# Kernel tuning notes

Measured on AMD Instinct MI355X. Metric: run time of the kernel, lower is better.

## Reference

```python
import jax, jax.numpy as jnp
import numpy as np

T, B, D, H, L = 512, 128, 256, 256, 4
EPS = 1e-5

def _ln(x, g, b):
    m = jnp.mean(x, axis=-1, keepdims=True)
    v = jnp.mean((x - m) ** 2, axis=-1, keepdims=True)
    return (x - m) * jax.lax.rsqrt(v + EPS) * g + b

def setup_inputs() -> dict:
    key = jax.random.key(0)
    ks = jax.random.split(key, 24)
    s = 0.02
    inp = {
        "x": jax.random.normal(ks[0], (T, B, D), dtype=jnp.float32),
        "lengths": jax.random.randint(ks[1], (B,), 1, T + 1, dtype=jnp.int32),
        # LinearEnchancedGRU params
        "Wr": jax.random.normal(ks[2], (D + H, H)) * s,
        "gr": jnp.ones((H,)), "br": jnp.zeros((H,)),
        "Wz": jax.random.normal(ks[3], (D + H, H)) * s,
        "gz": jnp.ones((H,)), "bz": jnp.zeros((H,)),
        "Wl": jax.random.normal(ks[4], (D + H, H)) * s,
        "gl": jnp.ones((H,)), "bl": jnp.zeros((H,)),
        "Wlt": jax.random.normal(ks[5], (D, H)) * s,
        "Cx": jax.random.normal(ks[6], (D, H)) * s,
        "Ch_w": jax.random.normal(ks[7], (H, H)) * s,
        "Ch_b": jnp.zeros((H,)),
        # TransitionGRU stack params [L, ...]
        "tWr": jax.random.normal(ks[8], (L, H, H)) * s,
        "tgr": jnp.ones((L, H)), "tbr": jnp.zeros((L, H)),
        "tWz": jax.random.normal(ks[9], (L, H, H)) * s,
        "tgz": jnp.ones((L, H)), "tbz": jnp.zeros((L, H)),
        "tWc": jax.random.normal(ks[10], (L, H, H)) * s,
        "tbc": jnp.zeros((L, H)),
    }
    return inp

def reference(x, lengths, Wr, gr, br, Wz, gz, bz, Wl, gl, bl, Wlt, Cx, Ch_w, Ch_b,
              tWr, tgr, tbr, tWz, tgz, tbz, tWc, tbc):
    # x: [T,B,D]; lengths: [B]. Packed-sequence semantics: hidden state of a
    # finished example is frozen; its outputs are zero padding.
    mask = jnp.arange(T, dtype=jnp.int32)[:, None] < lengths[None, :]  # [T,B]

    def cell(xt, h):
        cat = jnp.concatenate([xt, h], axis=-1)  # [B, D+H]
        r = jax.nn.sigmoid(_ln(cat @ Wr, gr, br))
        z = jax.nn.sigmoid(_ln(cat @ Wz, gz, bz))
        l = jax.nn.sigmoid(_ln(cat @ Wl, gl, bl))
        n = jnp.tanh(xt @ Cx + r * (h @ Ch_w + Ch_b)) + l * (xt @ Wlt)
        h = (1.0 - z) * h + z * n
        for i in range(L):  # deep transition stack (fixed small depth)
            ri = jax.nn.sigmoid(_ln(h @ tWr[i], tgr[i], tbr[i]))
            zi = jax.nn.sigmoid(_ln(h @ tWz[i], tgz[i], tbz[i]))
            ni = jnp.tanh(ri * (h @ tWc[i] + tbc[i]))
            h = (1.0 - zi) * ni + zi * h
        return h

    def step(h, inputs):
        xt, mt = inputs  # [B,D], [B]
        hn = cell(xt, h)
        hn = jnp.where(mt[:, None], hn, h)
        out = jnp.where(mt[:, None], hn, 0.0)
        return hn, out

    h0 = jnp.zeros((B, H), dtype=x.dtype)
    _, outs = jax.lax.scan(step, h0, (x, mask))  # outs: [T,B,H]
    return outs
```

## Files before the change

kernel.cpp:

```cpp
#include <hip/hip_runtime.h>
#include <hip/hip_bf16.h>

#define T_ 512
#define B_ 128
#define D_ 256
#define H_ 256
#define EPS 1e-5f

typedef __attribute__((ext_vector_type(8))) short short8;
typedef __attribute__((ext_vector_type(4))) short short4v;
typedef __attribute__((ext_vector_type(4))) float f32x4;
typedef __attribute__((ext_vector_type(4))) unsigned u32x4;
typedef unsigned long long ull;

#define SLICE_E  86016
#define WT_TOTAL 1376256

#define STATS_OFFB 2752512UL
#define HX_OFFB    2850816UL
#define FLAG_OFFB  3112960UL
#define SYNC0_OFFB HX_OFFB
#define SYNC0_BYTES (262144UL + 1024UL)

#define L_XBF  0
#define L_HBF  8192
#define L_G6   16384
#define L_SRED 22528
#define L_AUX  23040
#define L_TRN  47616
#define L_END  145920

__device__ __forceinline__ short f2bf(float f) {
  unsigned u = __builtin_bit_cast(unsigned, f);
  u = (u + 0x7FFFu + ((u >> 16) & 1u)) >> 16;
  return (short)u;
}
__device__ __forceinline__ f32x4 zero4() { f32x4 z = {0.f, 0.f, 0.f, 0.f}; return z; }
__device__ __forceinline__ f32x4 mfma16(short8 a, short8 b, f32x4 c) {
  return __builtin_amdgcn_mfma_f32_16x16x32_bf16(a, b, c, 0, 0, 0);
}
__device__ __forceinline__ void waitv0() { asm volatile("s_waitcnt vmcnt(0)" ::: "memory"); }

__device__ __forceinline__ f32x4 ald4(float* p) {
  ull* q = (ull*)p;
  ull a = __hip_atomic_load(q,     __ATOMIC_RELAXED, __HIP_MEMORY_SCOPE_AGENT);
  ull b = __hip_atomic_load(q + 1, __ATOMIC_RELAXED, __HIP_MEMORY_SCOPE_AGENT);
  f32x4 v;
  v[0] = __builtin_bit_cast(float, (unsigned)(a & 0xffffffffu));
  v[1] = __builtin_bit_cast(float, (unsigned)(a >> 32));
  v[2] = __builtin_bit_cast(float, (unsigned)(b & 0xffffffffu));
  v[3] = __builtin_bit_cast(float, (unsigned)(b >> 32));
  return v;
}
__device__ __forceinline__ void ast1f(float* p, float v) {
  __hip_atomic_store((unsigned*)p, __builtin_bit_cast(unsigned, v),
                     __ATOMIC_RELAXED, __HIP_MEMORY_SCOPE_AGENT);
}
__device__ __forceinline__ ull ald8(ull* p) {
  return __hip_atomic_load(p, __ATOMIC_RELAXED, __HIP_MEMORY_SCOPE_AGENT);
}
__device__ __forceinline__ void ast8(ull* p, ull v) {
  __hip_atomic_store(p, v, __ATOMIC_RELAXED, __HIP_MEMORY_SCOPE_AGENT);
}

__global__ void prep_weights(const float* __restrict__ Wr, const float* __restrict__ Wz,
                             const float* __restrict__ Wl, const float* __restrict__ Wlt,
                             const float* __restrict__ Cx, const float* __restrict__ Chw,
                             const float* __restrict__ tWr, const float* __restrict__ tWz,
                             const float* __restrict__ tWc, short* __restrict__ wt) {
  int idx = blockIdx.x * 256 + threadIdx.x;
  if (idx >= WT_TOTAL) return;
  int j  = idx / SLICE_E;
  int r  = idx - j * SLICE_E;
  int u  = r >> 12;
  int rr = r & 4095;
  int kf = rr >> 9;
  int le = rr & 511;
  int l  = le >> 3, e = le & 7;
  int la = l & 15, lh = l >> 4;
  int col = j * 16 + la;
  float v;
  if (u < 6) {
    int g = u >> 1, half = u & 1;
    int k = half * 256 + lh * 8 + kf * 32 + e;
    const float* W = (g == 0) ? Wr : (g == 1 ? Wz : Wl);
    v = W[k * 256 + col];
  } else if (u < 9) {
    int a = u - 6;
    int k = lh * 8 + kf * 32 + e;
    const float* W = (a == 0) ? Cx : (a == 1 ? Wlt : Chw);
    v = W[k * 256 + col];
  } else {
    int q = u - 9;
    int li = q / 3, m = q - li * 3;
    int k = lh * 8 + kf * 32 + e;
    const float* W = (m == 0) ? tWr : (m == 1 ? tWz : tWc);
    v = W[(li * 256 + k) * 256 + col];
  }
  wt[idx] = f2bf(v);
}

__global__ __launch_bounds__(64)
void rnn_sx(const float* __restrict__ x, const int* __restrict__ lengths,
            const float* __restrict__ gr, const float* __restrict__ br,
            const float* __restrict__ gz, const float* __restrict__ bz,
            const float* __restrict__ gl, const float* __restrict__ bl,
            const float* __restrict__ Chb,
            const float* __restrict__ tgr, const float* __restrict__ tbr,
            const float* __restrict__ tgz, const float* __restrict__ tbz,
            const float* __restrict__ tbc,
            const short* __restrict__ W, float* __restrict__ stats,
            ull* __restrict__ hx8, unsigned* __restrict__ flags,
            float* __restrict__ out) {

  __shared__ __align__(16) char smem[L_END];

  const int l  = threadIdx.x;
  const int la = l & 15, lh = l >> 4;
  const int amask = (la & 7) << 4;
  const int bid = blockIdx.x;
  const int cl = bid & 7, j = bid >> 3;
  const int rb0 = cl * 16;
  const int myrow = l >> 2, mc = (l & 3) * 4;
  const int cg = j * 16 + mc;
  const int colb = (l & 3) * 64;

  const short* Wsl = W + (size_t)j * SLICE_E;

  #pragma unroll 1
  for (int u = 0; u < 15; ++u) {
    char* dst = smem + ((u < 3) ? (L_AUX + u * 8192) : (L_TRN + (u - 3) * 8192));
    const short* src = Wsl + (size_t)(u + 6) * 4096;
    #pragma unroll
    for (int kf = 0; kf < 8; ++kf)
      *(short8*)(dst + kf * 1024 + l * 16) = *(const short8*)(src + kf * 512 + l * 8);
  }
  for (int i = l; i < 1024; i += 64) ((short4v*)(smem + L_HBF))[i] = (short4v){0, 0, 0, 0};

  int maxlen = 0;
  for (int i = 0; i < 16; ++i) {
    int v = lengths[rb0 + i];
    maxlen = maxlen > v ? maxlen : v;
  }
  const int mylen = lengths[rb0 + myrow];

  float* stc = stats + (size_t)(cl * 2) * 1536;
  ull*   hxc = hx8 + (size_t)cl * 4096;
  unsigned* flc = flags + cl * 32;

  f32x4 hreg = zero4();
  int dead = 0;

  auto pollf = [&](int par, unsigned tag) {
    if (!dead && l < 16) {
      unsigned* sp = flc + par * 16 + l;
      int it = 0;
      while (__hip_atomic_load(sp, __ATOMIC_RELAXED, __HIP_MEMORY_SCOPE_AGENT) < tag) {
        if (++it > 300000) { dead = 1; break; }
        if (it > 4) __builtin_amdgcn_s_sleep(1);
      }
    }
    asm volatile("" ::: "memory");
  };
  auto ldu = [&](short8 (&dst)[8], const short* bp) {
    #pragma unroll
    for (int kf = 0; kf < 8; ++kf) dst[kf] = *(const short8*)(bp + kf * 512 + l * 8);
  };
  auto mm8r = [&](short8 (&Bv)[8], f32x4& acc, int Ab) {
    #pragma unroll
    for (int kf = 0; kf < 8; ++kf) {
      int aoff = Ab + la * 512 + (((kf * 64) + lh * 16) ^ amask);
      acc = mfma16(*(const short8*)(smem + aoff), Bv[kf], acc);
    }
  };
  auto mmlds = [&](int Bub, f32x4& acc, int Ab) {
    #pragma unroll
    for (int kf = 0; kf < 8; ++kf) {
      int aoff = Ab + la * 512 + (((kf * 64) + lh * 16) ^ amask);
      short8 bv = *(const short8*)(smem + Bub + kf * 1024 + l * 16);
      acc = mfma16(*(const short8*)(smem + aoff), bv, acc);
    }
  };
  auto g6store = [&](int arr, f32x4 acc) {
    #pragma unroll
    for (int i = 0; i < 4; ++i)
      *(float*)(smem + L_G6 + ((arr * 16 + lh * 4 + i) * 16 + la) * 4) = acc[i];
  };
  auto posth = [&](int par, unsigned tag) {
    unsigned lo0 = (unsigned)(unsigned short)f2bf(hreg[0]) |
                   ((unsigned)(unsigned short)f2bf(hreg[1]) << 16);
    unsigned lo1 = (unsigned)(unsigned short)f2bf(hreg[2]) |
                   ((unsigned)(unsigned short)f2bf(hreg[3]) << 16);
    ull* hp = hxc + par * 2048 + myrow * 128 + j * 8 + (l & 3) * 2;
    ast8(hp,     (ull)lo0 | ((ull)tag << 32));
    ast8(hp + 1, (ull)lo1 | ((ull)tag << 32));
  };
  auto readhx = [&](int par, unsigned tag) {
    int row2 = l >> 2;
    ull* hp = hxc + par * 2048 + row2 * 128 + (l & 3) * 32;
    unsigned lo[32];
    bool ok = false;
    int it = 0;
    for (;;) {
      if (!ok) {
        unsigned mn = 0xffffffffu;
        #pragma unroll
        for (int k = 0; k < 32; ++k) {
          ull v = ald8(hp + k);
          lo[k] = (unsigned)v;
          unsigned tg = (unsigned)(v >> 32);
          mn = mn < tg ? mn : tg;
        }
        ok = (mn >= tag);
      }
      if (__all((int)ok) || dead) break;
      if (++it > 100000) dead = 1;
      if (it > 4) __builtin_amdgcn_s_sleep(1);
    }
    #pragma unroll
    for (int q = 0; q < 8; ++q) {
      u32x4 v = { lo[4 * q], lo[4 * q + 1], lo[4 * q + 2], lo[4 * q + 3] };
      *(u32x4*)(smem + L_HBF + row2 * 512 + (((l & 3) * 128 + q * 16) ^ ((row2 & 7) << 4))) = v;
    }
  };

  short8 B0[8], B1[8];
  ldu(B0, Wsl);
  ldu(B1, Wsl + 4096);

  for (int t = 0; t < maxlen; ++t) {
    int R = t * 5, par = R & 1;
    unsigned tag = (unsigned)(R + 1);
    {
      const float* xs = x + ((size_t)t * B_ + rb0 + (l >> 2)) * D_ + colb;
      int row2 = l >> 2;
      #pragma unroll
      for (int u2 = 0; u2 < 8; ++u2) {
        f32x4 a = *(const f32x4*)(xs + u2 * 8);
        f32x4 b = *(const f32x4*)(xs + u2 * 8 + 4);
        short8 s;
        s[0] = f2bf(a[0]); s[1] = f2bf(a[1]); s[2] = f2bf(a[2]); s[3] = f2bf(a[3]);
        s[4] = f2bf(b[0]); s[5] = f2bf(b[1]); s[6] = f2bf(b[2]); s[7] = f2bf(b[3]);
        *(short8*)(smem + L_XBF + row2 * 512 + ((colb * 2 + u2 * 16) ^ ((row2 & 7) << 4))) = s;
      }
    }
    f32x4 ac[6];
    #pragma unroll
    for (int a2 = 0; a2 < 6; ++a2) ac[a2] = zero4();
    mm8r(B0, ac[0], L_XBF); ldu(B0, Wsl + 2 * 4096);
    mm8r(B1, ac[0], L_HBF); ldu(B1, Wsl + 3 * 4096);
    mm8r(B0, ac[1], L_XBF); ldu(B0, Wsl + 4 * 4096);
    mm8r(B1, ac[1], L_HBF); ldu(B1, Wsl + 5 * 4096);
    mm8r(B0, ac[2], L_XBF);
    mm8r(B1, ac[2], L_HBF);
    mmlds(L_AUX,         ac[3], L_XBF);
    mmlds(L_AUX + 8192,  ac[4], L_XBF);
    mmlds(L_AUX + 16384, ac[5], L_HBF);
    #pragma unroll
    for (int a2 = 0; a2 < 6; ++a2) g6store(a2, ac[a2]);
    f32x4 pv[6];
    #pragma unroll
    for (int a2 = 0; a2 < 6; ++a2)
      pv[a2] = *(const f32x4*)(smem + L_G6 + ((a2 * 16 + myrow) * 16 + mc) * 4);
    float st[6];
    #pragma unroll
    for (int g2 = 0; g2 < 3; ++g2) {
      f32x4 v = pv[g2];
      st[2 * g2]     = v[0] + v[1] + v[2] + v[3];
      st[2 * g2 + 1] = v[0] * v[0] + v[1] * v[1] + v[2] * v[2] + v[3] * v[3];
    }
    #pragma unroll
    for (int s2 = 0; s2 < 6; ++s2) {
      st[s2] += __shfl_xor(st[s2], 1);
      st[s2] += __shfl_xor(st[s2], 2);
    }
    float* sp = stc + par * 1536;
    {
      int k4 = l & 3;
      ast1f(sp + (k4 * 16 + myrow) * 16 + j, st[k4]);
      if (k4 < 2) ast1f(sp + ((4 + k4) * 16 + myrow) * 16 + j, st[4 + k4]);
    }
    waitv0();
    if (l == 0)
      __hip_atomic_store(flc + par * 16 + j, tag, __ATOMIC_RELAXED, __HIP_MEMORY_SCOPE_AGENT);
    pollf(par, tag);
    {
      float* q = sp + l * 16;
      f32x4 a = ald4(q), b = ald4(q + 4), c = ald4(q + 8), d = ald4(q + 12);
      f32x4 s4 = a + b + c + d;
      *(float*)(smem + L_SRED + l * 4) = s4[0] + s4[1] + s4[2] + s4[3];
      if (l < 32) {
        float* q2 = sp + (64 + l) * 16;
        f32x4 a2 = ald4(q2), b2 = ald4(q2 + 4), c2 = ald4(q2 + 8), d2 = ald4(q2 + 12);
        f32x4 t4 = a2 + b2 + c2 + d2;
        *(float*)(smem + L_SRED + (64 + l) * 4) = t4[0] + t4[1] + t4[2] + t4[3];
      }
    }
    {
      float m3[3], rs3[3];
      #pragma unroll
      for (int g2 = 0; g2 < 3; ++g2) {
        float s1 = *(float*)(smem + L_SRED + ((2 * g2) * 16 + myrow) * 4);
        float s2 = *(float*)(smem + L_SRED + ((2 * g2 + 1) * 16 + myrow) * 4);
        float mm = s1 * (1.f / 256.f);
        float vv = s2 * (1.f / 256.f) - mm * mm;
        m3[g2] = mm; rs3[g2] = rsqrtf((vv > 0.f ? vv : 0.f) + EPS);
      }
      f32x4 g4r = *(const f32x4*)(gr + cg), b4r = *(const f32x4*)(br + cg);
      f32x4 g4z = *(const f32x4*)(gz + cg), b4z = *(const f32x4*)(bz + cg);
      f32x4 g4l = *(const f32x4*)(gl + cg), b4l = *(const f32x4*)(bl + cg);
      f32x4 cb4 = *(const f32x4*)(Chb + cg);
      bool act = t < mylen;
      f32x4 hn;
      #pragma unroll
      for (int q2 = 0; q2 < 4; ++q2) {
        float rv = 1.f / (1.f + __expf(-((pv[0][q2] - m3[0]) * rs3[0] * g4r[q2] + b4r[q2])));
        float zv = 1.f / (1.f + __expf(-((pv[1][q2] - m3[1]) * rs3[1] * g4z[q2] + b4z[q2])));
        float lv = 1.f / (1.f + __expf(-((pv[2][q2] - m3[2]) * rs3[2] * g4l[q2] + b4l[q2])));
        float n = tanhf(pv[3][q2] + rv * (pv[5][q2] + cb4[q2])) + lv * pv[4][q2];
        hn[q2] = (1.f - zv) * hreg[q2] + zv * n;
      }
      if (act) hreg = hn;
    }
    posth(par, tag);
    readhx(par, tag);

    #pragma unroll 1
    for (int li = 0; li < 4; ++li) {
      R = t * 5 + 1 + li; par = R & 1; tag = (unsigned)(R + 1);
      f32x4 tc0 = zero4(), tc1 = zero4(), tc2 = zero4();
      mmlds(L_TRN + (li * 3 + 0) * 8192, tc0, L_HBF);
      mmlds(L_TRN + (li * 3 + 1) * 8192, tc1, L_HBF);
      mmlds(L_TRN + (li * 3 + 2) * 8192, tc2, L_HBF);
      g6store(0, tc0); g6store(1, tc1); g6store(2, tc2);
      f32x4 qv[3];
      #pragma unroll
      for (int a2 = 0; a2 < 3; ++a2)
        qv[a2] = *(const f32x4*)(smem + L_G6 + ((a2 * 16 + myrow) * 16 + mc) * 4);
      float st4[4];
      #pragma unroll
      for (int g2 = 0; g2 < 2; ++g2) {
        f32x4 v = qv[g2];
        st4[2 * g2]     = v[0] + v[1] + v[2] + v[3];
        st4[2 * g2 + 1] = v[0] * v[0] + v[1] * v[1] + v[2] * v[2] + v[3] * v[3];
      }
      #pragma unroll
      for (int s2 = 0; s2 < 4; ++s2) {
        st4[s2] += __shfl_xor(st4[s2], 1);
        st4[s2] += __shfl_xor(st4[s2], 2);
      }
      float* sp2 = stc + par * 1536;
      ast1f(sp2 + ((l & 3) * 16 + myrow) * 16 + j, st4[l & 3]);
      waitv0();
      if (l == 0)
        __hip_atomic_store(flc + par * 16 + j, tag, __ATOMIC_RELAXED, __HIP_MEMORY_SCOPE_AGENT);
      if (li == 3) {
        ldu(B0, Wsl);
        ldu(B1, Wsl + 4096);
      }
      pollf(par, tag);
      {
        float* q = sp2 + l * 16;
        f32x4 a = ald4(q), b = ald4(q + 4), c = ald4(q + 8), d = ald4(q + 12);
        f32x4 s4 = a + b + c + d;
        *(float*)(smem + L_SRED + l * 4) = s4[0] + s4[1] + s4[2] + s4[3];
      }
      bool act = t < mylen;
      {
        float m2[2], rs2[2];
        #pragma unroll
        for (int g2 = 0; g2 < 2; ++g2) {
          float s1 = *(float*)(smem + L_SRED + ((2 * g2) * 16 + myrow) * 4);
          float s2 = *(float*)(smem + L_SRED + ((2 * g2 + 1) * 16 + myrow) * 4);
          float mm = s1 * (1.f / 256.f);
          float vv = s2 * (1.f / 256.f) - mm * mm;
          m2[g2] = mm; rs2[g2] = rsqrtf((vv > 0.f ? vv : 0.f) + EPS);
        }
        f32x4 g4r = *(const f32x4*)(tgr + li * 256 + cg), b4r = *(const f32x4*)(tbr + li * 256 + cg);
        f32x4 g4z = *(const f32x4*)(tgz + li * 256 + cg), b4z = *(const f32x4*)(tbz + li * 256 + cg);
        f32x4 cb4 = *(const f32x4*)(tbc + li * 256 + cg);
        f32x4 hn;
        #pragma unroll
        for (int q2 = 0; q2 < 4; ++q2) {
          float rv = 1.f / (1.f + __expf(-((qv[0][q2] - m2[0]) * rs2[0] * g4r[q2] + b4r[q2])));
          float zv = 1.f / (1.f + __expf(-((qv[1][q2] - m2[1]) * rs2[1] * g4z[q2] + b4z[q2])));
          float n = tanhf(rv * (qv[2][q2] + cb4[q2]));
          hn[q2] = (1.f - zv) * n + zv * hreg[q2];
        }
        if (act) hreg = hn;
        if (li == 3) {
          f32x4 o = act ? hreg : zero4();
          *(f32x4*)(out + ((size_t)t * B_ + rb0 + myrow) * H_ + cg) = o;
        }
      }
      posth(par, tag);
      readhx(par, tag);
    }
  }

  for (int t2 = maxlen; t2 < T_; ++t2)
    *(f32x4*)(out + ((size_t)t2 * B_ + rb0 + myrow) * H_ + cg) = zero4();
}

extern "C" void kernel_launch(void* const* d_in, const int* in_sizes, int n_in,
                              void* d_out, int out_size, void* d_ws, size_t ws_size,
                              hipStream_t stream) {
  const float* x    = (const float*)d_in[0];
  const int* lengths = (const int*)d_in[1];
  const float* Wr   = (const float*)d_in[2];
  const float* gr   = (const float*)d_in[3];
  const float* br   = (const float*)d_in[4];
  const float* Wz   = (const float*)d_in[5];
  const float* gz   = (const float*)d_in[6];
  const float* bz   = (const float*)d_in[7];
  const float* Wl   = (const float*)d_in[8];
  const float* gl   = (const float*)d_in[9];
  const float* bl   = (const float*)d_in[10];
  const float* Wlt  = (const float*)d_in[11];
  const float* Cx   = (const float*)d_in[12];
  const float* Chw  = (const float*)d_in[13];
  const float* Chb  = (const float*)d_in[14];
  const float* tWr  = (const float*)d_in[15];
  const float* tgr  = (const float*)d_in[16];
  const float* tbr  = (const float*)d_in[17];
  const float* tWz  = (const float*)d_in[18];
  const float* tgz  = (const float*)d_in[19];
  const float* tbz  = (const float*)d_in[20];
  const float* tWc  = (const float*)d_in[21];
  const float* tbc  = (const float*)d_in[22];

  short*    wt    = (short*)d_ws;
  float*    stats = (float*)((char*)d_ws + STATS_OFFB);
  ull*      hx8   = (ull*)((char*)d_ws + HX_OFFB);
  unsigned* flags = (unsigned*)((char*)d_ws + FLAG_OFFB);

  hipMemsetAsync((char*)d_ws + SYNC0_OFFB, 0, SYNC0_BYTES, stream);
  hipLaunchKernelGGL(prep_weights, dim3((WT_TOTAL + 255) / 256), dim3(256), 0, stream,
                     Wr, Wz, Wl, Wlt, Cx, Chw, tWr, tWz, tWc, wt);
  hipLaunchKernelGGL(rnn_sx, dim3(128), dim3(64), 0, stream,
                     x, lengths, gr, br, gz, bz, gl, bl, Chb,
                     tgr, tbr, tgz, tbz, tbc, wt, stats, hx8, flags, (float*)d_out);
}
```

Before: 17.89 ms.

## Exchange fp16 pre-activations instead of hidden state, one barrier per layer

Each block now publishes its fp16-packed matmul pre-activations and LayerNorm partial stats to global memory behind a single flag barrier. After the barrier, every block redundantly reads all blocks' pre-activations and computes the full hidden state for its 16 rows locally in LDS. The second tagged hidden-state exchange and its polling loop per layer are gone, which halves the cross-block sync rounds per sub-step. In exchange each block does 16x more elementwise gate math and global reads, and fp16 rounding of the pre-activations adds precision risk.

Result: slower. 53.26 ms (+197.7%).

```diff
diff --git a/kernel.cpp b/kernel.cpp
--- a/kernel.cpp
+++ b/kernel.cpp
@@ -10,37 +10,41 @@
 typedef __attribute__((ext_vector_type(8))) short short8;
 typedef __attribute__((ext_vector_type(4))) short short4v;
 typedef __attribute__((ext_vector_type(4))) float f32x4;
-typedef __attribute__((ext_vector_type(4))) unsigned u32x4;
 typedef unsigned long long ull;
 
 #define SLICE_E  86016
 #define WT_TOTAL 1376256
 
-#define STATS_OFFB 2752512UL
-#define HX_OFFB    2850816UL
-#define FLAG_OFFB  3112960UL
-#define SYNC0_OFFB HX_OFFB
-#define SYNC0_BYTES (262144UL + 1024UL)
+#define PRE_OFFB   2752512UL
+#define STATS_OFFB 3538944UL
+#define FLAG_OFFB  3637248UL
+#define FLAG_BYTES 1024UL
 
 #define L_XBF  0
 #define L_HBF  8192
-#define L_G6   16384
-#define L_SRED 22528
-#define L_AUX  23040
-#define L_TRN  47616
-#define L_END  145920
+#define L_HF   16384
+#define L_SRED 32768
+#define L_AUX  33280
+#define L_TRN  57856
+#define L_END  156160
 
 __device__ __forceinline__ short f2bf(float f) {
   unsigned u = __builtin_bit_cast(unsigned, f);
   u = (u + 0x7FFFu + ((u >> 16) & 1u)) >> 16;
   return (short)u;
 }
+__device__ __forceinline__ unsigned short f2h(float f) {
+  _Float16 h = (_Float16)f;
+  return __builtin_bit_cast(unsigned short, h);
+}
+__device__ __forceinline__ float h2f(unsigned short u) {
+  return (float)__builtin_bit_cast(_Float16, u);
+}
 __device__ __forceinline__ f32x4 zero4() { f32x4 z = {0.f, 0.f, 0.f, 0.f}; return z; }
 __device__ __forceinline__ f32x4 mfma16(short8 a, short8 b, f32x4 c) {
   return __builtin_amdgcn_mfma_f32_16x16x32_bf16(a, b, c, 0, 0, 0);
 }
 __device__ __forceinline__ void waitv0() { asm volatile("s_waitcnt vmcnt(0)" ::: "memory"); }
-
 __device__ __forceinline__ f32x4 ald4(float* p) {
   ull* q = (ull*)p;
   ull a = __hip_atomic_load(q,     __ATOMIC_RELAXED, __HIP_MEMORY_SCOPE_AGENT);
@@ -61,6 +65,13 @@
 }
 __device__ __forceinline__ void ast8(ull* p, ull v) {
   __hip_atomic_store(p, v, __ATOMIC_RELAXED, __HIP_MEMORY_SCOPE_AGENT);
+}
+__device__ __forceinline__ ull pack4h(f32x4 v) {
+  return (ull)f2h(v[0]) | ((ull)f2h(v[1]) << 16) | ((ull)f2h(v[2]) << 32) |
+         ((ull)f2h(v[3]) << 48);
+}
+__device__ __forceinline__ int hfoff(int row, int cb4) {
+  return L_HF + row * 1024 + ((cb4 * 16) ^ ((((row & 7) ^ (cb4 >> 2)) & 7) << 4));
 }
 
 __global__ void prep_weights(const float* __restrict__ Wr, const float* __restrict__ Wz,
@@ -101,7 +112,7 @@
 }
 
 __global__ __launch_bounds__(64)
-void rnn_sx(const float* __restrict__ x, const int* __restrict__ lengths,
+void rnn_1c(const float* __restrict__ x, const int* __restrict__ lengths,
             const float* __restrict__ gr, const float* __restrict__ br,
             const float* __restrict__ gz, const float* __restrict__ bz,
             const float* __restrict__ gl, const float* __restrict__ bl,
@@ -109,8 +120,8 @@
             const float* __restrict__ tgr, const float* __restrict__ tbr,
             const float* __restrict__ tgz, const float* __restrict__ tbz,
             const float* __restrict__ tbc,
-            const short* __restrict__ W, float* __restrict__ stats,
-            ull* __restrict__ hx8, unsigned* __restrict__ flags,
+            const short* __restrict__ W, ull* __restrict__ pre8,
+            float* __restrict__ stats, unsigned* __restrict__ flags,
             float* __restrict__ out) {
 
   __shared__ __align__(16) char smem[L_END];
@@ -121,8 +132,6 @@
   const int bid = blockIdx.x;
   const int cl = bid & 7, j = bid >> 3;
   const int rb0 = cl * 16;
-  const int myrow = l >> 2, mc = (l & 3) * 4;
-  const int cg = j * 16 + mc;
   const int colb = (l & 3) * 64;
 
   const short* Wsl = W + (size_t)j * SLICE_E;
@@ -136,19 +145,20 @@
       *(short8*)(dst + kf * 1024 + l * 16) = *(const short8*)(src + kf * 512 + l * 8);
   }
   for (int i = l; i < 1024; i += 64) ((short4v*)(smem + L_HBF))[i] = (short4v){0, 0, 0, 0};
+  for (int i = l; i < 1024; i += 64) ((f32x4*)(smem + L_HF))[i] = zero4();
 
   int maxlen = 0;
   for (int i = 0; i < 16; ++i) {
     int v = lengths[rb0 + i];
     maxlen = maxlen > v ? maxlen : v;
   }
-  const int mylen = lengths[rb0 + myrow];
-
-  float* stc = stats + (size_t)(cl * 2) * 1536;
-  ull*   hxc = hx8 + (size_t)cl * 4096;
+  int lenr[4];
+  #pragma unroll
+  for (int i = 0; i < 4; ++i) lenr[i] = lengths[rb0 + lh * 4 + i];
+
+  ull*   preB0 = pre8 + (size_t)cl * 12288;
+  float* stc   = stats + (size_t)cl * 3072;
   unsigned* flc = flags + cl * 32;
-
-  f32x4 hreg = zero4();
   int dead = 0;
 
   auto pollf = [&](int par, unsigned tag) {
@@ -181,46 +191,26 @@
       acc = mfma16(*(const short8*)(smem + aoff), bv, acc);
     }
   };
-  auto g6store = [&](int arr, f32x4 acc) {
-    #pragma unroll
-    for (int i = 0; i < 4; ++i)
-      *(float*)(smem + L_G6 + ((arr * 16 + lh * 4 + i) * 16 + la) * 4) = acc[i];
-  };
-  auto posth = [&](int par, unsigned tag) {
-    unsigned lo0 = (unsigned)(unsigned short)f2bf(hreg[0]) |
-                   ((unsigned)(unsigned short)f2bf(hreg[1]) << 16);
-    unsigned lo1 = (unsigned)(unsigned short)f2bf(hreg[2]) |
-                   ((unsigned)(unsigned short)f2bf(hreg[3]) << 16);
-    ull* hp = hxc + par * 2048 + myrow * 128 + j * 8 + (l & 3) * 2;
-    ast8(hp,     (ull)lo0 | ((ull)tag << 32));
-    ast8(hp + 1, (ull)lo1 | ((ull)tag << 32));
-  };
-  auto readhx = [&](int par, unsigned tag) {
-    int row2 = l >> 2;
-    ull* hp = hxc + par * 2048 + row2 * 128 + (l & 3) * 32;
-    unsigned lo[32];
-    bool ok = false;
-    int it = 0;
-    for (;;) {
-      if (!ok) {
-        unsigned mn = 0xffffffffu;
-        #pragma unroll
-        for (int k = 0; k < 32; ++k) {
-          ull v = ald8(hp + k);
-          lo[k] = (unsigned)v;
-          unsigned tg = (unsigned)(v >> 32);
-          mn = mn < tg ? mn : tg;
-        }
-        ok = (mn >= tag);
-      }
-      if (__all((int)ok) || dead) break;
-      if (++it > 100000) dead = 1;
-      if (it > 4) __builtin_amdgcn_s_sleep(1);
-    }
-    #pragma unroll
-    for (int q = 0; q < 8; ++q) {
-      u32x4 v = { lo[4 * q], lo[4 * q + 1], lo[4 * q + 2], lo[4 * q + 3] };
-      *(u32x4*)(smem + L_HBF + row2 * 512 + (((l & 3) * 128 + q * 16) ^ ((row2 & 7) << 4))) = v;
+  auto statpost = [&](float* sp, int slotg, int i, float a) {
+    float b = a * a;
+    a += __shfl_xor(a, 1); b += __shfl_xor(b, 1);
+    a += __shfl_xor(a, 2); b += __shfl_xor(b, 2);
+    a += __shfl_xor(a, 4); b += __shfl_xor(b, 4);
+    a += __shfl_xor(a, 8); b += __shfl_xor(b, 8);
+    int row = lh * 4 + i;
+    if (la == 2 * i)     ast1f(sp + ((2 * slotg) * 16 + row) * 16 + j, a);
+    if (la == 2 * i + 1) ast1f(sp + ((2 * slotg + 1) * 16 + row) * 16 + j, b);
+  };
+  auto redstats = [&](float* sp, bool both) {
+    float* q = sp + l * 16;
+    f32x4 a = ald4(q), b = ald4(q + 4), c = ald4(q + 8), d = ald4(q + 12);
+    f32x4 s4 = a + b + c + d;
+    *(float*)(smem + L_SRED + l * 4) = s4[0] + s4[1] + s4[2] + s4[3];
+    if (both && l < 32) {
+      float* q2 = sp + (64 + l) * 16;
+      f32x4 a2 = ald4(q2), b2 = ald4(q2 + 4), c2 = ald4(q2 + 8), d2 = ald4(q2 + 12);
+      f32x4 t4 = a2 + b2 + c2 + d2;
+      *(float*)(smem + L_SRED + (64 + l) * 4) = t4[0] + t4[1] + t4[2] + t4[3];
     }
   };
 
@@ -229,177 +219,189 @@
   ldu(B1, Wsl + 4096);
 
   for (int t = 0; t < maxlen; ++t) {
-    int R = t * 5, par = R & 1;
-    unsigned tag = (unsigned)(R + 1);
     {
-      const float* xs = x + ((size_t)t * B_ + rb0 + (l >> 2)) * D_ + colb;
-      int row2 = l >> 2;
-      #pragma unroll
-      for (int u2 = 0; u2 < 8; ++u2) {
-        f32x4 a = *(const f32x4*)(xs + u2 * 8);
-        f32x4 b = *(const f32x4*)(xs + u2 * 8 + 4);
-        short8 s;
-        s[0] = f2bf(a[0]); s[1] = f2bf(a[1]); s[2] = f2bf(a[2]); s[3] = f2bf(a[3]);
-        s[4] = f2bf(b[0]); s[5] = f2bf(b[1]); s[6] = f2bf(b[2]); s[7] = f2bf(b[3]);
-        *(short8*)(smem + L_XBF + row2 * 512 + ((colb * 2 + u2 * 16) ^ ((row2 & 7) << 4))) = s;
+      int R = t * 5, par = R & 1;
+      unsigned tag = (unsigned)(R + 1);
+      ull* preB = preB0 + par * 6144;
+      float* sp = stc + par * 1536;
+      {
+        const float* xs = x + ((size_t)t * B_ + rb0 + (l >> 2)) * D_ + colb;
+        int row2 = l >> 2;
+        #pragma unroll
+        for (int u2 = 0; u2 < 8; ++u2) {
+          f32x4 a = *(const f32x4*)(xs + u2 * 8);
+          f32x4 b = *(const f32x4*)(xs + u2 * 8 + 4);
+          short8 s;
+          s[0] = f2bf(a[0]); s[1] = f2bf(a[1]); s[2] = f2bf(a[2]); s[3] = f2bf(a[3]);
+          s[4] = f2bf(b[0]); s[5] = f2bf(b[1]); s[6] = f2bf(b[2]); s[7] = f2bf(b[3]);
+          *(short8*)(smem + L_XBF + row2 * 512 + ((colb * 2 + u2 * 16) ^ ((row2 & 7) << 4))) = s;
+        }
       }
-    }
-    f32x4 ac[6];
-    #pragma unroll
-    for (int a2 = 0; a2 < 6; ++a2) ac[a2] = zero4();
-    mm8r(B0, ac[0], L_XBF); ldu(B0, Wsl + 2 * 4096);
-    mm8r(B1, ac[0], L_HBF); ldu(B1, Wsl + 3 * 4096);
-    mm8r(B0, ac[1], L_XBF); ldu(B0, Wsl + 4 * 4096);
-    mm8r(B1, ac[1], L_HBF); ldu(B1, Wsl + 5 * 4096);
-    mm8r(B0, ac[2], L_XBF);
-    mm8r(B1, ac[2], L_HBF);
-    mmlds(L_AUX,         ac[3], L_XBF);
-    mmlds(L_AUX + 8192,  ac[4], L_XBF);
-    mmlds(L_AUX + 16384, ac[5], L_HBF);
-    #pragma unroll
-    for (int a2 = 0; a2 < 6; ++a2) g6store(a2, ac[a2]);
-    f32x4 pv[6];
-    #pragma unroll
-    for (int a2 = 0; a2 < 6; ++a2)
-      pv[a2] = *(const f32x4*)(smem + L_G6 + ((a2 * 16 + myrow) * 16 + mc) * 4);
-    float st[6];
-    #pragma unroll
-    for (int g2 = 0; g2 < 3; ++g2) {
-      f32x4 v = pv[g2];
-      st[2 * g2]     = v[0] + v[1] + v[2] + v[3];
-      st[2 * g2 + 1] = v[0] * v[0] + v[1] * v[1] + v[2] * v[2] + v[3] * v[3];
-    }
-    #pragma unroll
-    for (int s2 = 0; s2 < 6; ++s2) {
-      st[s2] += __shfl_xor(st[s2], 1);
-      st[s2] += __shfl_xor(st[s2], 2);
-    }
-    float* sp = stc + par * 1536;
-    {
-      int k4 = l & 3;
-      ast1f(sp + (k4 * 16 + myrow) * 16 + j, st[k4]);
-      if (k4 < 2) ast1f(sp + ((4 + k4) * 16 + myrow) * 16 + j, st[4 + k4]);
-    }
-    waitv0();
-    if (l == 0)
-      __hip_atomic_store(flc + par * 16 + j, tag, __ATOMIC_RELAXED, __HIP_MEMORY_SCOPE_AGENT);
-    pollf(par, tag);
-    {
-      float* q = sp + l * 16;
-      f32x4 a = ald4(q), b = ald4(q + 4), c = ald4(q + 8), d = ald4(q + 12);
-      f32x4 s4 = a + b + c + d;
-      *(float*)(smem + L_SRED + l * 4) = s4[0] + s4[1] + s4[2] + s4[3];
-      if (l < 32) {
-        float* q2 = sp + (64 + l) * 16;
-        f32x4 a2 = ald4(q2), b2 = ald4(q2 + 4), c2 = ald4(q2 + 8), d2 = ald4(q2 + 12);
-        f32x4 t4 = a2 + b2 + c2 + d2;
-        *(float*)(smem + L_SRED + (64 + l) * 4) = t4[0] + t4[1] + t4[2] + t4[3];
-      }
-    }
-    {
-      float m3[3], rs3[3];
-      #pragma unroll
-      for (int g2 = 0; g2 < 3; ++g2) {
-        float s1 = *(float*)(smem + L_SRED + ((2 * g2) * 16 + myrow) * 4);
-        float s2 = *(float*)(smem + L_SRED + ((2 * g2 + 1) * 16 + myrow) * 4);
-        float mm = s1 * (1.f / 256.f);
-        float vv = s2 * (1.f / 256.f) - mm * mm;
-        m3[g2] = mm; rs3[g2] = rsqrtf((vv > 0.f ? vv : 0.f) + EPS);
-      }
-      f32x4 g4r = *(const f32x4*)(gr + cg), b4r = *(const f32x4*)(br + cg);
-      f32x4 g4z = *(const f32x4*)(gz + cg), b4z = *(const f32x4*)(bz + cg);
-      f32x4 g4l = *(const f32x4*)(gl + cg), b4l = *(const f32x4*)(bl + cg);
-      f32x4 cb4 = *(const f32x4*)(Chb + cg);
-      bool act = t < mylen;
-      f32x4 hn;
-      #pragma unroll
-      for (int q2 = 0; q2 < 4; ++q2) {
-        float rv = 1.f / (1.f + __expf(-((pv[0][q2] - m3[0]) * rs3[0] * g4r[q2] + b4r[q2])));
-        float zv = 1.f / (1.f + __expf(-((pv[1][q2] - m3[1]) * rs3[1] * g4z[q2] + b4z[q2])));
-        float lv = 1.f / (1.f + __expf(-((pv[2][q2] - m3[2]) * rs3[2] * g4l[q2] + b4l[q2])));
-        float n = tanhf(pv[3][q2] + rv * (pv[5][q2] + cb4[q2])) + lv * pv[4][q2];
-        hn[q2] = (1.f - zv) * hreg[q2] + zv * n;
-      }
-      if (act) hreg = hn;
-    }
-    posth(par, tag);
-    readhx(par, tag);
-
-    #pragma unroll 1
-    for (int li = 0; li < 4; ++li) {
-      R = t * 5 + 1 + li; par = R & 1; tag = (unsigned)(R + 1);
-      f32x4 tc0 = zero4(), tc1 = zero4(), tc2 = zero4();
-      mmlds(L_TRN + (li * 3 + 0) * 8192, tc0, L_HBF);
-      mmlds(L_TRN + (li * 3 + 1) * 8192, tc1, L_HBF);
-      mmlds(L_TRN + (li * 3 + 2) * 8192, tc2, L_HBF);
-      g6store(0, tc0); g6store(1, tc1); g6store(2, tc2);
-      f32x4 qv[3];
-      #pragma unroll
-      for (int a2 = 0; a2 < 3; ++a2)
-        qv[a2] = *(const f32x4*)(smem + L_G6 + ((a2 * 16 + myrow) * 16 + mc) * 4);
-      float st4[4];
-      #pragma unroll
-      for (int g2 = 0; g2 < 2; ++g2) {
-        f32x4 v = qv[g2];
-        st4[2 * g2]     = v[0] + v[1] + v[2] + v[3];
-        st4[2 * g2 + 1] = v[0] * v[0] + v[1] * v[1] + v[2] * v[2] + v[3] * v[3];
-      }
-      #pragma unroll
-      for (int s2 = 0; s2 < 4; ++s2) {
-        st4[s2] += __shfl_xor(st4[s2], 1);
-        st4[s2] += __shfl_xor(st4[s2], 2);
-      }
-      float* sp2 = stc + par * 1536;
-      ast1f(sp2 + ((l & 3) * 16 + myrow) * 16 + j, st4[l & 3]);
+      f32x4 ac[6];
+      #pragma unroll
+      for (int a2 = 0; a2 < 6; ++a2) ac[a2] = zero4();
+      mm8r(B0, ac[0], L_XBF); ldu(B0, Wsl + 2 * 4096);
+      mm8r(B1, ac[0], L_HBF); ldu(B1, Wsl + 3 * 4096);
+      mm8r(B0, ac[1], L_XBF); ldu(B0, Wsl + 4 * 4096);
+      mm8r(B1, ac[1], L_HBF); ldu(B1, Wsl + 5 * 4096);
+      mm8r(B0, ac[2], L_XBF);
+      mm8r(B1, ac[2], L_HBF);
+      mmlds(L_AUX,         ac[3], L_XBF);
+      mmlds(L_AUX + 8192,  ac[4], L_XBF);
+      mmlds(L_AUX + 16384, ac[5], L_HBF);
+      #pragma unroll
+      for (int arr = 0; arr < 6; ++arr)
+        ast8(preB + ((arr * 4 + lh) << 8) + j * 16 + la, pack4h(ac[arr]));
+      #pragma unroll
+      for (int g2 = 0; g2 < 3; ++g2)
+        #pragma unroll
+        for (int i = 0; i < 4; ++i) statpost(sp, g2, i, ac[g2][i]);
       waitv0();
       if (l == 0)
         __hip_atomic_store(flc + par * 16 + j, tag, __ATOMIC_RELAXED, __HIP_MEMORY_SCOPE_AGENT);
-      if (li == 3) {
-        ldu(B0, Wsl);
-        ldu(B1, Wsl + 4096);
-      }
       pollf(par, tag);
-      {
-        float* q = sp2 + l * 16;
-        f32x4 a = ald4(q), b = ald4(q + 4), c = ald4(q + 8), d = ald4(q + 12);
-        f32x4 s4 = a + b + c + d;
-        *(float*)(smem + L_SRED + l * 4) = s4[0] + s4[1] + s4[2] + s4[3];
-      }
-      bool act = t < mylen;
-      {
-        float m2[2], rs2[2];
-        #pragma unroll
-        for (int g2 = 0; g2 < 2; ++g2) {
-          float s1 = *(float*)(smem + L_SRED + ((2 * g2) * 16 + myrow) * 4);
-          float s2 = *(float*)(smem + L_SRED + ((2 * g2 + 1) * 16 + myrow) * 4);
+      redstats(sp, true);
+      float mG[3][4], rG[3][4];
+      #pragma unroll
+      for (int g2 = 0; g2 < 3; ++g2)
+        #pragma unroll
+        for (int i = 0; i < 4; ++i) {
+          int row = lh * 4 + i;
+          float s1 = *(float*)(smem + L_SRED + ((2 * g2) * 16 + row) * 4);
+          float s2 = *(float*)(smem + L_SRED + ((2 * g2 + 1) * 16 + row) * 4);
           float mm = s1 * (1.f / 256.f);
           float vv = s2 * (1.f / 256.f) - mm * mm;
-          m2[g2] = mm; rs2[g2] = rsqrtf((vv > 0.f ? vv : 0.f) + EPS);
+          mG[g2][i] = mm; rG[g2][i] = rsqrtf((vv > 0.f ? vv : 0.f) + EPS);
         }
-        f32x4 g4r = *(const f32x4*)(tgr + li * 256 + cg), b4r = *(const f32x4*)(tbr + li * 256 + cg);
-        f32x4 g4z = *(const f32x4*)(tgz + li * 256 + cg), b4z = *(const f32x4*)(tbz + li * 256 + cg);
-        f32x4 cb4 = *(const f32x4*)(tbc + li * 256 + cg);
-        f32x4 hn;
-        #pragma unroll
-        for (int q2 = 0; q2 < 4; ++q2) {
-          float rv = 1.f / (1.f + __expf(-((qv[0][q2] - m2[0]) * rs2[0] * g4r[q2] + b4r[q2])));
-          float zv = 1.f / (1.f + __expf(-((qv[1][q2] - m2[1]) * rs2[1] * g4z[q2] + b4z[q2])));
-          float n = tanhf(rv * (qv[2][q2] + cb4[q2]));
-          hn[q2] = (1.f - zv) * n + zv * hreg[q2];
-        }
-        if (act) hreg = hn;
-        if (li == 3) {
-          f32x4 o = act ? hreg : zero4();
-          *(f32x4*)(out + ((size_t)t * B_ + rb0 + myrow) * H_ + cg) = o;
+      #pragma unroll
+      for (int c = 0; c < 4; ++c) {
+        ull q[6][4];
+        #pragma unroll
+        for (int arr = 0; arr < 6; ++arr)
+          #pragma unroll
+          for (int k = 0; k < 4; ++k)
+            q[arr][k] = ald8(preB + ((arr * 4 + lh) << 8) + la * 16 + c * 4 + k);
+        int c0g = la * 16 + c * 4;
+        f32x4 g4r = *(const f32x4*)(gr + c0g), b4r = *(const f32x4*)(br + c0g);
+        f32x4 g4z = *(const f32x4*)(gz + c0g), b4z = *(const f32x4*)(bz + c0g);
+        f32x4 g4l = *(const f32x4*)(gl + c0g), b4l = *(const f32x4*)(bl + c0g);
+        f32x4 cb4 = *(const f32x4*)(Chb + c0g);
+        #pragma unroll
+        for (int i = 0; i < 4; ++i) {
+          int row = lh * 4 + i;
+          int ho = hfoff(row, la * 4 + c);
+          f32x4 hold = *(const f32x4*)(smem + ho);
+          bool act = t < lenr[i];
+          f32x4 hn;
+          #pragma unroll
+          for (int k = 0; k < 4; ++k) {
+            float P0 = h2f((unsigned short)(q[0][k] >> (16 * i)));
+            float P1 = h2f((unsigned short)(q[1][k] >> (16 * i)));
+            float P2 = h2f((unsigned short)(q[2][k] >> (16 * i)));
+            float P3 = h2f((unsigned short)(q[3][k] >> (16 * i)));
+            float P4 = h2f((unsigned short)(q[4][k] >> (16 * i)));
+            float P5 = h2f((unsigned short)(q[5][k] >> (16 * i)));
+            float rv = 1.f / (1.f + __expf(-((P0 - mG[0][i]) * rG[0][i] * g4r[k] + b4r[k])));
+            float zv = 1.f / (1.f + __expf(-((P1 - mG[1][i]) * rG[1][i] * g4z[k] + b4z[k])));
+            float lv = 1.f / (1.f + __expf(-((P2 - mG[2][i]) * rG[2][i] * g4l[k] + b4l[k])));
+            float n  = tanhf(P3 + rv * (P5 + cb4[k])) + lv * P4;
+            float hv = (1.f - zv) * hold[k] + zv * n;
+            hn[k] = act ? hv : hold[k];
+          }
+          *(f32x4*)(smem + ho) = hn;
+          short4v sv = { f2bf(hn[0]), f2bf(hn[1]), f2bf(hn[2]), f2bf(hn[3]) };
+          *(short4v*)(smem + L_HBF + row * 512 + ((la * 32 + c * 8) ^ ((row & 7) << 4))) = sv;
         }
       }
-      posth(par, tag);
-      readhx(par, tag);
+    }
+
+    #pragma unroll 1
+    for (int li = 0; li < 4; ++li) {
+      int R = t * 5 + 1 + li, par = R & 1;
+      unsigned tag = (unsigned)(R + 1);
+      ull* preB = preB0 + par * 6144;
+      float* sp = stc + par * 1536;
+      f32x4 tc[3];
+      #pragma unroll
+      for (int a2 = 0; a2 < 3; ++a2) tc[a2] = zero4();
+      mmlds(L_TRN + (li * 3 + 0) * 8192, tc[0], L_HBF);
+      mmlds(L_TRN + (li * 3 + 1) * 8192, tc[1], L_HBF);
+      mmlds(L_TRN + (li * 3 + 2) * 8192, tc[2], L_HBF);
+      #pragma unroll
+      for (int arr = 0; arr < 3; ++arr)
+        ast8(preB + ((arr * 4 + lh) << 8) + j * 16 + la, pack4h(tc[arr]));
+      #pragma unroll
+      for (int g2 = 0; g2 < 2; ++g2)
+        #pragma unroll
+        for (int i = 0; i < 4; ++i) statpost(sp, g2, i, tc[g2][i]);
+      waitv0();
+      if (l == 0)
+        __hip_atomic_store(flc + par * 16 + j, tag, __ATOMIC_RELAXED, __HIP_MEMORY_SCOPE_AGENT);
+      if (li == 3) { ldu(B0, Wsl); ldu(B1, Wsl + 4096); }
+      pollf(par, tag);
+      redstats(sp, false);
+      float mT[2][4], rT[2][4];
+      #pragma unroll
+      for (int g2 = 0; g2 < 2; ++g2)
+        #pragma unroll
+        for (int i = 0; i < 4; ++i) {
+          int row = lh * 4 + i;
+          float s1 = *(float*)(smem + L_SRED + ((2 * g2) * 16 + row) * 4);
+          float s2 = *(float*)(smem + L_SRED + ((2 * g2 + 1) * 16 + row) * 4);
+          float mm = s1 * (1.f / 256.f);
+          float vv = s2 * (1.f / 256.f) - mm * mm;
+          mT[g2][i] = mm; rT[g2][i] = rsqrtf((vv > 0.f ? vv : 0.f) + EPS);
+        }
+      #pragma unroll
+      for (int c = 0; c < 4; ++c) {
+        ull q[3][4];
+        #pragma unroll
+        for (int arr = 0; arr < 3; ++arr)
+          #pragma unroll
+          for (int k = 0; k < 4; ++k)
+            q[arr][k] = ald8(preB + ((arr * 4 + lh) << 8) + la * 16 + c * 4 + k);
+        int c0g = la * 16 + c * 4;
+        f32x4 g4r = *(const f32x4*)(tgr + li * 256 + c0g), b4r = *(const f32x4*)(tbr + li * 256 + c0g);
+        f32x4 g4z = *(const f32x4*)(tgz + li * 256 + c0g), b4z = *(const f32x4*)(tbz + li * 256 + c0g);
+        f32x4 cb4 = *(const f32x4*)(tbc + li * 256 + c0g);
+        #pragma unroll
+        for (int i = 0; i < 4; ++i) {
+          int row = lh * 4 + i;
+          int ho = hfoff(row, la * 4 + c);
+          f32x4 hold = *(const f32x4*)(smem + ho);
+          bool act = t < lenr[i];
+          f32x4 hn;
+          #pragma unroll
+          for (int k = 0; k < 4; ++k) {
+            float P0 = h2f((unsigned short)(q[0][k] >> (16 * i)));
+            float P1 = h2f((unsigned short)(q[1][k] >> (16 * i)));
+            float P2 = h2f((unsigned short)(q[2][k] >> (16 * i)));
+            float rv = 1.f / (1.f + __expf(-((P0 - mT[0][i]) * rT[0][i] * g4r[k] + b4r[k])));
+            float zv = 1.f / (1.f + __expf(-((P1 - mT[1][i]) * rT[1][i] * g4z[k] + b4z[k])));
+            float n  = tanhf(rv * (P2 + cb4[k]));
+            float hv = (1.f - zv) * n + zv * hold[k];
+            hn[k] = act ? hv : hold[k];
+          }
+          *(f32x4*)(smem + ho) = hn;
+          short4v sv = { f2bf(hn[0]), f2bf(hn[1]), f2bf(hn[2]), f2bf(hn[3]) };
+          *(short4v*)(smem + L_HBF + row * 512 + ((la * 32 + c * 8) ^ ((row & 7) << 4))) = sv;
+          if (li == 3 && la == j) {
+            f32x4 o;
+            #pragma unroll
+            for (int k = 0; k < 4; ++k) o[k] = act ? hn[k] : 0.f;
+            *(f32x4*)(out + ((size_t)t * B_ + rb0 + row) * H_ + c0g) = o;
+          }
+        }
+      }
     }
   }
 
-  for (int t2 = maxlen; t2 < T_; ++t2)
-    *(f32x4*)(out + ((size_t)t2 * B_ + rb0 + myrow) * H_ + cg) = zero4();
+  {
+    const int myrow = l >> 2, mc = (l & 3) * 4;
+    const int cg = j * 16 + mc;
+    for (int t2 = maxlen; t2 < T_; ++t2)
+      *(f32x4*)(out + ((size_t)t2 * B_ + rb0 + myrow) * H_ + cg) = zero4();
+  }
 }
 
 extern "C" void kernel_launch(void* const* d_in, const int* in_sizes, int n_in,
@@ -430,14 +432,14 @@
   const float* tbc  = (const float*)d_in[22];
 
   short*    wt    = (short*)d_ws;
+  ull*      pre8  = (ull*)((char*)d_ws + PRE_OFFB);
   float*    stats = (float*)((char*)d_ws + STATS_OFFB);
-  ull*      hx8   = (ull*)((char*)d_ws + HX_OFFB);
   unsigned* flags = (unsigned*)((char*)d_ws + FLAG_OFFB);
 
-  hipMemsetAsync((char*)d_ws + SYNC0_OFFB, 0, SYNC0_BYTES, stream);
+  hipMemsetAsync(flags, 0, FLAG_BYTES, stream);
   hipLaunchKernelGGL(prep_weights, dim3((WT_TOTAL + 255) / 256), dim3(256), 0, stream,
                      Wr, Wz, Wl, Wlt, Cx, Chw, tWr, tWz, tWc, wt);
-  hipLaunchKernelGGL(rnn_sx, dim3(128), dim3(64), 0, stream,
+  hipLaunchKernelGGL(rnn_1c, dim3(128), dim3(64), 0, stream,
                      x, lengths, gr, br, gz, bz, gl, bl, Chb,
-                     tgr, tbr, tgz, tbz, tbc, wt, stats, hx8, flags, (float*)d_out);
-}
+                     tgr, tbr, tgz, tbz, tbc, wt, pre8, stats, flags, (float*)d_out);
+}
```
